# Kernel optimization log

Hardware: AMD Instinct MI355X
Metric: run time of the kernel (lower is better)

The kernel has to match this reference:

```python
import jax, jax.numpy as jnp
import numpy as np

EPS = 1e-12  # matches torch F.normalize default eps

def setup_inputs() -> dict:
    key = jax.random.key(0)
    k1, k2 = jax.random.split(key)
    n, d = 8192, 1024
    x = jax.random.normal(k1, (n, d), dtype=jnp.float32)
    weight = jax.random.normal(k2, (d, d), dtype=jnp.float32) * (2.0 / d) ** 0.5
    return {"x": x, "weight": weight}

def reference(x, weight):
    # L2-normalize rows (torch F.normalize, dim=1): x / max(||x||_2, eps)
    nrm = jnp.sqrt(jnp.sum(x * x, axis=1, keepdims=True))
    norm = x / jnp.maximum(nrm, EPS)
    # adjacency: cosine-similarity Gram matrix [n, n] (materialized as in source)
    adj = norm @ norm.T
    ax = adj @ x          # [n, d]
    axw = ax @ weight     # [n, d]
    return axw
```

## Files before the change

### kernel.cpp

```cpp
#include <hip/hip_runtime.h>
#include <stdint.h>

typedef unsigned short u16;
typedef unsigned int u32;
typedef __attribute__((ext_vector_type(8))) short short8;
typedef __attribute__((ext_vector_type(4))) float floatx4;

__device__ __forceinline__ u16 f2b(float f) {
    u32 u = __builtin_bit_cast(u32, f);
    return (u16)((u + 0x7fffu + ((u >> 16) & 1u)) >> 16);
}

__device__ __forceinline__ void gld16(const void* g, void* l) {
    __builtin_amdgcn_global_load_lds(
        (const __attribute__((address_space(1))) u32*)g,
        (__attribute__((address_space(3))) u32*)l, 16, 0, 0);
}

__global__ __launch_bounds__(256) void prep_norms(
    const float* __restrict__ x, float* __restrict__ rnorm, float* __restrict__ srnorm) {
    int row = blockIdx.x;
    int t = threadIdx.x;
    float4 v = ((const float4*)(x + (long)row * 1024))[t];
    float ss = v.x * v.x + v.y * v.y + v.z * v.z + v.w * v.w;
    #pragma unroll
    for (int off = 32; off > 0; off >>= 1) ss += __shfl_down(ss, off);
    __shared__ float red[4];
    if ((t & 63) == 0) red[t >> 6] = ss;
    __syncthreads();
    if (t == 0) {
        float r = 1.0f / fmaxf(sqrtf(red[0] + red[1] + red[2] + red[3]), 1e-12f);
        rnorm[row] = r;
        srnorm[row] = sqrtf(r);
    }
}

__global__ __launch_bounds__(256) void transpose_scale_dual(
    const float* __restrict__ src, const float* __restrict__ sr,
    u16* __restrict__ dstT, u16* __restrict__ dstR, int rows, int cols) {
    __shared__ float tile[64][65];
    __shared__ float rbuf[64];
    int r0 = blockIdx.x * 64, c0 = blockIdx.y * 64;
    int t = threadIdx.x;
    if (t < 64) rbuf[t] = (sr != nullptr) ? sr[r0 + t] : 1.0f;
    __syncthreads();
    #pragma unroll
    for (int i = 0; i < 4; i++) {
        int lin = i * 256 + t;
        int rr = lin >> 4, c4 = (lin & 15) << 2;
        float4 v = *(const float4*)(src + (long)(r0 + rr) * cols + c0 + c4);
        float s = rbuf[rr];
        v.x *= s; v.y *= s; v.z *= s; v.w *= s;
        tile[rr][c4] = v.x; tile[rr][c4 + 1] = v.y; tile[rr][c4 + 2] = v.z; tile[rr][c4 + 3] = v.w;
        if (dstR != nullptr) {
            ushort4 o; o.x = f2b(v.x); o.y = f2b(v.y); o.z = f2b(v.z); o.w = f2b(v.w);
            *(ushort4*)(dstR + (long)(r0 + rr) * cols + c0 + c4) = o;
        }
    }
    __syncthreads();
    #pragma unroll
    for (int i = 0; i < 4; i++) {
        int lin = i * 256 + t;
        int cc = lin >> 4, r4 = (lin & 15) << 2;
        ushort4 o;
        o.x = f2b(tile[r4][cc]);
        o.y = f2b(tile[r4 + 1][cc]);
        o.z = f2b(tile[r4 + 2][cc]);
        o.w = f2b(tile[r4 + 3][cc]);
        *(ushort4*)(dstT + (long)(c0 + cc) * rows + r0 + r4) = o;
    }
}

__global__ __launch_bounds__(256) void reduce_cast(
    const float* __restrict__ P, u16* __restrict__ D, int S, long E) {
    long i = ((long)blockIdx.x * 256 + threadIdx.x) * 4;
    float4 s = *(const float4*)(P + i);
    for (int z = 1; z < S; z++) {
        float4 v = *(const float4*)(P + z * E + i);
        s.x += v.x; s.y += v.y; s.z += v.z; s.w += v.w;
    }
    ushort4 o;
    o.x = f2b(s.x); o.y = f2b(s.y); o.z = f2b(s.z); o.w = f2b(s.w);
    *(ushort4*)(D + i) = o;
}

__global__ __launch_bounds__(256) void reduce_sym64(
    const float* __restrict__ P, u16* __restrict__ D, int S, long E) {
    __shared__ float lt[64][65];
    int ti = blockIdx.x >> 4, tj = blockIdx.x & 15;
    int t = threadIdx.x;
    int r = t >> 4, c4 = (t & 15) << 2;
    int kept = (ti <= 2 * (tj >> 1) + 1);
    if (kept) {
        #pragma unroll
        for (int it = 0; it < 4; it++) {
            int row = 64 * ti + it * 16 + r;
            long idx = (long)row * 1024 + 64 * tj + c4;
            float4 s = *(const float4*)(P + idx);
            for (int z = 1; z < S; z++) {
                float4 v = *(const float4*)(P + (long)z * E + idx);
                s.x += v.x; s.y += v.y; s.z += v.z; s.w += v.w;
            }
            ushort4 o; o.x = f2b(s.x); o.y = f2b(s.y); o.z = f2b(s.z); o.w = f2b(s.w);
            *(ushort4*)(D + idx) = o;
        }
    } else {
        #pragma unroll
        for (int it = 0; it < 4; it++) {
            int row = it * 16 + r;
            long idx = (long)(64 * tj + row) * 1024 + 64 * ti + c4;
            float4 s = *(const float4*)(P + idx);
            for (int z = 1; z < S; z++) {
                float4 v = *(const float4*)(P + (long)z * E + idx);
                s.x += v.x; s.y += v.y; s.z += v.z; s.w += v.w;
            }
            lt[row][c4] = s.x; lt[row][c4 + 1] = s.y; lt[row][c4 + 2] = s.z; lt[row][c4 + 3] = s.w;
        }
        __syncthreads();
        #pragma unroll
        for (int it = 0; it < 4; it++) {
            int dr = it * 16 + r;
            ushort4 o;
            o.x = f2b(lt[c4 + 0][dr]); o.y = f2b(lt[c4 + 1][dr]);
            o.z = f2b(lt[c4 + 2][dr]); o.w = f2b(lt[c4 + 3][dr]);
            *(ushort4*)(D + (long)(64 * ti + dr) * 1024 + 64 * tj + c4) = o;
        }
    }
}

__global__ __launch_bounds__(256, 4) void gemm64x128(
    const u16* __restrict__ A, const u16* __restrict__ B,
    float* __restrict__ C, const float* __restrict__ rowscale,
    int lda, int ldb, int ldc, int tilesN, int kIters, long coffz, int sym) {
    __shared__ __align__(16) u16 As[64 * 64];
    __shared__ __align__(16) u16 Bs[128 * 64];
    int tm, tn;
    if (sym) {
        int id = blockIdx.x, j = 0;
        while (true) {
            int c = (2 * j + 2 < 16) ? (2 * j + 2) : 16;
            if (id < c) break;
            id -= c; j++;
        }
        tn = j; tm = id;
    } else {
        tm = blockIdx.x / tilesN; tn = blockIdx.x % tilesN;
    }
    long kOff = (long)blockIdx.y * kIters * 64;
    const u16* Ap = A + (long)tm * 64 * lda + kOff;
    const u16* Bp = B + (long)tn * 128 * ldb + kOff;
    long coff = (long)blockIdx.y * coffz;

    int t = threadIdx.x;
    int lane = t & 63, w = t >> 6;
    int wm = (w & 1) * 32, wn = (w >> 1) * 64;
    int r16 = lane & 15, q = lane >> 4;

    int acl[2], bcl[4];
    #pragma unroll
    for (int j = 0; j < 2; j++) acl[j] = (w * 2 + j) * 64 + lane;
    #pragma unroll
    for (int j = 0; j < 4; j++) bcl[j] = (w * 4 + j) * 64 + lane;

    floatx4 acc[2][4];
    #pragma unroll
    for (int i = 0; i < 2; i++)
        #pragma unroll
        for (int j = 0; j < 4; j++) acc[i][j] = (floatx4){0.f, 0.f, 0.f, 0.f};

    for (int kt = 0; kt < kIters; kt++) {
        long kk = (long)kt * 64;
        #pragma unroll
        for (int j = 0; j < 2; j++) {
            int cl = acl[j], row = cl >> 3, cg = (cl & 7) ^ (row & 7);
            gld16(Ap + (long)row * lda + kk + cg * 8, (void*)&As[cl * 8]);
        }
        #pragma unroll
        for (int j = 0; j < 4; j++) {
            int cl = bcl[j], row = cl >> 3, cg = (cl & 7) ^ (row & 7);
            gld16(Bp + (long)row * ldb + kk + cg * 8, (void*)&Bs[cl * 8]);
        }
        __syncthreads();
        #pragma unroll
        for (int ks = 0; ks < 2; ks++) {
            short8 a[2], b[4];
            #pragma unroll
            for (int i = 0; i < 2; i++) {
                int rr = wm + i * 16 + r16;
                int cc = (ks * 4 + q) ^ (rr & 7);
                a[i] = *(const short8*)&As[rr * 64 + cc * 8];
            }
            #pragma unroll
            for (int j = 0; j < 4; j++) {
                int rr = wn + j * 16 + r16;
                int cc = (ks * 4 + q) ^ (rr & 7);
                b[j] = *(const short8*)&Bs[rr * 64 + cc * 8];
            }
            #pragma unroll
            for (int i = 0; i < 2; i++)
                #pragma unroll
                for (int j = 0; j < 4; j++)
                    acc[i][j] = __builtin_amdgcn_mfma_f32_16x16x32_bf16(a[i], b[j], acc[i][j], 0, 0, 0);
        }
        __syncthreads();
    }

    int m0 = tm * 64 + wm, n0 = tn * 128 + wn;
    #pragma unroll
    for (int i = 0; i < 2; i++) {
        int mm = m0 + i * 16 + q * 4;
        float rs[4];
        #pragma unroll
        for (int r = 0; r < 4; r++) rs[r] = (rowscale != nullptr) ? rowscale[mm + r] : 1.0f;
        #pragma unroll
        for (int j = 0; j < 4; j++) {
            int nn = n0 + j * 16 + r16;
            #pragma unroll
            for (int r = 0; r < 4; r++)
                C[coff + (long)(mm + r) * ldc + nn] = acc[i][j][r] * rs[r];
        }
    }
}

extern "C" void kernel_launch(void* const* d_in, const int* in_sizes, int n_in,
                              void* d_out, int out_size, void* d_ws, size_t ws_size,
                              hipStream_t stream) {
    const float* x = (const float*)d_in[0];
    const float* wgt = (const float*)d_in[1];
    float* out = (float*)d_out;
    char* ws = (char*)d_ws;

    const size_t MB = 1048576;
    float* rnorm  = (float*)ws;
    float* srnorm = (float*)(ws + 32768);
    u16*   YT     = (u16*)(ws + 65536);
    u16*   Yb     = (u16*)(ws + 65536 + 16 * MB);
    u16*   Wt     = (u16*)(ws + 65536 + 32 * MB);
    u16*   Gb     = (u16*)(ws + 65536 + 34 * MB);
    u16*   Mt     = (u16*)(ws + 65536 + 36 * MB);
    float* Gp     = (float*)(ws + 65536 + 38 * MB);
    float* Mp     = (float*)(ws + 65536 + 70 * MB);

    prep_norms<<<8192, 256, 0, stream>>>(x, rnorm, srnorm);
    transpose_scale_dual<<<dim3(128, 16), 256, 0, stream>>>(x, srnorm, YT, Yb, 8192, 1024);
    transpose_scale_dual<<<dim3(16, 16), 256, 0, stream>>>(wgt, nullptr, Wt, nullptr, 1024, 1024);
    gemm64x128<<<dim3(72, 8), 256, 0, stream>>>(YT, YT, Gp, nullptr,
                                                8192, 8192, 1024, 8, 16, 1048576, 1);
    reduce_sym64<<<256, 256, 0, stream>>>(Gp, Gb, 8, 1048576);
    gemm64x128<<<dim3(128, 2), 256, 0, stream>>>(Wt, Gb, Mp, nullptr,
                                                 1024, 1024, 1024, 8, 8, 1048576, 0);
    reduce_cast<<<1024, 256, 0, stream>>>(Mp, Mt, 2, 1048576);
    gemm64x128<<<dim3(1024, 1), 256, 0, stream>>>(Yb, Mt, out, srnorm,
                                                  1024, 1024, 1024, 8, 16, 0, 0);
}
```

Measured before the change: 168.1 us.

## Fuse norm prep, drop split-K reduce, add 128x128 final GEMM and block swizzle

Merges the row-norm pass and the transpose/scale pass into a single kernel that writes both the transposed sqrt-scaled Y and the fully normalized row-major Yn. The W·G GEMM no longer uses split-K: it writes bf16 output directly, so the separate reduce_cast kernel is removed. The final GEMM becomes a new 128x128-tile kernel with no row scale, since the rows are already fully normalized. Both GEMMs get a block-index remap over groups of 8, likely aiming at better distribution across the chip's XCDs and cache locality. The trade-offs are a W·G GEMM that now runs only 128 blocks, and the fused prep kernel reading x twice with just 256 blocks.

```diff
diff --git a/kernel.cpp b/kernel.cpp
--- a/kernel.cpp
+++ b/kernel.cpp
@@ -17,21 +17,55 @@
         (__attribute__((address_space(3))) u32*)l, 16, 0, 0);
 }
 
-__global__ __launch_bounds__(256) void prep_norms(
-    const float* __restrict__ x, float* __restrict__ rnorm, float* __restrict__ srnorm) {
-    int row = blockIdx.x;
-    int t = threadIdx.x;
-    float4 v = ((const float4*)(x + (long)row * 1024))[t];
-    float ss = v.x * v.x + v.y * v.y + v.z * v.z + v.w * v.w;
-    #pragma unroll
-    for (int off = 32; off > 0; off >>= 1) ss += __shfl_down(ss, off);
-    __shared__ float red[4];
-    if ((t & 63) == 0) red[t >> 6] = ss;
-    __syncthreads();
-    if (t == 0) {
-        float r = 1.0f / fmaxf(sqrtf(red[0] + red[1] + red[2] + red[3]), 1e-12f);
-        rnorm[row] = r;
-        srnorm[row] = sqrtf(r);
+__global__ __launch_bounds__(256) void fuse_prep(
+    const float* __restrict__ x, u16* __restrict__ YT, u16* __restrict__ Yn) {
+    __shared__ float tile[32][129];
+    int r0 = blockIdx.x * 32;
+    int t = threadIdx.x;
+    int tg = t >> 5, tl = t & 31;
+    float ss[4] = {0.f, 0.f, 0.f, 0.f};
+    for (int c = 0; c < 8; c++) {
+        #pragma unroll
+        for (int i = 0; i < 4; i++) {
+            int rr = i * 8 + tg;
+            float4 v = *(const float4*)(x + (long)(r0 + rr) * 1024 + c * 128 + tl * 4);
+            ss[i] += v.x * v.x + v.y * v.y + v.z * v.z + v.w * v.w;
+        }
+    }
+    float rs_[4], sr_[4];
+    #pragma unroll
+    for (int i = 0; i < 4; i++) {
+        #pragma unroll
+        for (int m = 16; m > 0; m >>= 1) ss[i] += __shfl_xor(ss[i], m);
+        float rcp = 1.0f / fmaxf(sqrtf(ss[i]), 1e-12f);
+        rs_[i] = rcp;
+        sr_[i] = sqrtf(rcp);
+    }
+    for (int c = 0; c < 8; c++) {
+        __syncthreads();
+        #pragma unroll
+        for (int i = 0; i < 4; i++) {
+            int rr = i * 8 + tg;
+            float4 v = *(const float4*)(x + (long)(r0 + rr) * 1024 + c * 128 + tl * 4);
+            ushort4 o;
+            o.x = f2b(v.x * rs_[i]); o.y = f2b(v.y * rs_[i]);
+            o.z = f2b(v.z * rs_[i]); o.w = f2b(v.w * rs_[i]);
+            *(ushort4*)(Yn + (long)(r0 + rr) * 1024 + c * 128 + tl * 4) = o;
+            tile[rr][tl * 4 + 0] = v.x * sr_[i];
+            tile[rr][tl * 4 + 1] = v.y * sr_[i];
+            tile[rr][tl * 4 + 2] = v.z * sr_[i];
+            tile[rr][tl * 4 + 3] = v.w * sr_[i];
+        }
+        __syncthreads();
+        #pragma unroll
+        for (int i = 0; i < 4; i++) {
+            int lin = i * 256 + t;
+            int cc = lin >> 3, r4 = (lin & 7) << 2;
+            ushort4 o;
+            o.x = f2b(tile[r4 + 0][cc]); o.y = f2b(tile[r4 + 1][cc]);
+            o.z = f2b(tile[r4 + 2][cc]); o.w = f2b(tile[r4 + 3][cc]);
+            *(ushort4*)(YT + (long)(c * 128 + cc) * 8192 + r0 + r4) = o;
+        }
     }
 }
 
@@ -71,19 +105,6 @@
     }
 }
 
-__global__ __launch_bounds__(256) void reduce_cast(
-    const float* __restrict__ P, u16* __restrict__ D, int S, long E) {
-    long i = ((long)blockIdx.x * 256 + threadIdx.x) * 4;
-    float4 s = *(const float4*)(P + i);
-    for (int z = 1; z < S; z++) {
-        float4 v = *(const float4*)(P + z * E + i);
-        s.x += v.x; s.y += v.y; s.z += v.z; s.w += v.w;
-    }
-    ushort4 o;
-    o.x = f2b(s.x); o.y = f2b(s.y); o.z = f2b(s.z); o.w = f2b(s.w);
-    *(ushort4*)(D + i) = o;
-}
-
 __global__ __launch_bounds__(256) void reduce_sym64(
     const float* __restrict__ P, u16* __restrict__ D, int S, long E) {
     __shared__ float lt[64][65];
@@ -131,12 +152,15 @@
 __global__ __launch_bounds__(256, 4) void gemm64x128(
     const u16* __restrict__ A, const u16* __restrict__ B,
     float* __restrict__ C, const float* __restrict__ rowscale,
-    int lda, int ldb, int ldc, int tilesN, int kIters, long coffz, int sym) {
+    int lda, int ldb, int ldc, int tilesN, int kIters, long coffz, int sym, int obf16) {
     __shared__ __align__(16) u16 As[64 * 64];
     __shared__ __align__(16) u16 Bs[128 * 64];
+    int bid = blockIdx.x;
+    int nx = gridDim.x;
+    if ((nx & 7) == 0) { int cpx = nx >> 3; bid = (bid & 7) * cpx + (bid >> 3); }
     int tm, tn;
     if (sym) {
-        int id = blockIdx.x, j = 0;
+        int id = bid, j = 0;
         while (true) {
             int c = (2 * j + 2 < 16) ? (2 * j + 2) : 16;
             if (id < c) break;
@@ -144,7 +168,7 @@
         }
         tn = j; tm = id;
     } else {
-        tm = blockIdx.x / tilesN; tn = blockIdx.x % tilesN;
+        tm = bid / tilesN; tn = bid % tilesN;
     }
     long kOff = (long)blockIdx.y * kIters * 64;
     const u16* Ap = A + (long)tm * 64 * lda + kOff;
@@ -216,8 +240,89 @@
         for (int j = 0; j < 4; j++) {
             int nn = n0 + j * 16 + r16;
             #pragma unroll
+            for (int r = 0; r < 4; r++) {
+                float v = acc[i][j][r] * rs[r];
+                if (obf16) ((u16*)C)[coff + (long)(mm + r) * ldc + nn] = f2b(v);
+                else       C[coff + (long)(mm + r) * ldc + nn] = v;
+            }
+        }
+    }
+}
+
+__global__ __launch_bounds__(256) void gemm128(
+    const u16* __restrict__ A, const u16* __restrict__ B,
+    float* __restrict__ C, const float* __restrict__ rowscale,
+    int lda, int ldb, int ldc, int tilesN, int kIters) {
+    __shared__ __align__(16) u16 As[128 * 64];
+    __shared__ __align__(16) u16 Bs[128 * 64];
+    int bid = blockIdx.x;
+    int nx = gridDim.x;
+    if ((nx & 7) == 0) { int cpx = nx >> 3; bid = (bid & 7) * cpx + (bid >> 3); }
+    int tm = bid / tilesN, tn = bid % tilesN;
+    const u16* Ap = A + (long)tm * 128 * lda;
+    const u16* Bp = B + (long)tn * 128 * ldb;
+
+    int t = threadIdx.x;
+    int lane = t & 63, w = t >> 6;
+    int wm = (w & 1) * 64, wn = (w >> 1) * 64;
+    int r16 = lane & 15, q = lane >> 4;
+
+    floatx4 acc[4][4];
+    #pragma unroll
+    for (int i = 0; i < 4; i++)
+        #pragma unroll
+        for (int j = 0; j < 4; j++) acc[i][j] = (floatx4){0.f, 0.f, 0.f, 0.f};
+
+    for (int kt = 0; kt < kIters; kt++) {
+        long kk = (long)kt * 64;
+        #pragma unroll
+        for (int j = 0; j < 4; j++) {
+            int cl = j * 256 + t, row = cl >> 3, cg = (cl & 7) ^ (row & 7);
+            gld16(Ap + (long)row * lda + kk + cg * 8, (void*)&As[cl * 8]);
+        }
+        #pragma unroll
+        for (int j = 0; j < 4; j++) {
+            int cl = j * 256 + t, row = cl >> 3, cg = (cl & 7) ^ (row & 7);
+            gld16(Bp + (long)row * ldb + kk + cg * 8, (void*)&Bs[cl * 8]);
+        }
+        __syncthreads();
+        #pragma unroll
+        for (int ks = 0; ks < 2; ks++) {
+            short8 a[4], b[4];
+            #pragma unroll
+            for (int i = 0; i < 4; i++) {
+                int rr = wm + i * 16 + r16;
+                int cc = (ks * 4 + q) ^ (rr & 7);
+                a[i] = *(const short8*)&As[rr * 64 + cc * 8];
+            }
+            #pragma unroll
+            for (int j = 0; j < 4; j++) {
+                int rr = wn + j * 16 + r16;
+                int cc = (ks * 4 + q) ^ (rr & 7);
+                b[j] = *(const short8*)&Bs[rr * 64 + cc * 8];
+            }
+            #pragma unroll
+            for (int i = 0; i < 4; i++)
+                #pragma unroll
+                for (int j = 0; j < 4; j++)
+                    acc[i][j] = __builtin_amdgcn_mfma_f32_16x16x32_bf16(a[i], b[j], acc[i][j], 0, 0, 0);
+        }
+        __syncthreads();
+    }
+
+    int m0 = tm * 128 + wm, n0 = tn * 128 + wn;
+    #pragma unroll
+    for (int i = 0; i < 4; i++) {
+        int mm = m0 + i * 16 + q * 4;
+        float rs[4];
+        #pragma unroll
+        for (int r = 0; r < 4; r++) rs[r] = (rowscale != nullptr) ? rowscale[mm + r] : 1.0f;
+        #pragma unroll
+        for (int j = 0; j < 4; j++) {
+            int nn = n0 + j * 16 + r16;
+            #pragma unroll
             for (int r = 0; r < 4; r++)
-                C[coff + (long)(mm + r) * ldc + nn] = acc[i][j][r] * rs[r];
+                C[(long)(mm + r) * ldc + nn] = acc[i][j][r] * rs[r];
         }
     }
 }
@@ -231,25 +336,20 @@
     char* ws = (char*)d_ws;
 
     const size_t MB = 1048576;
-    float* rnorm  = (float*)ws;
-    float* srnorm = (float*)(ws + 32768);
-    u16*   YT     = (u16*)(ws + 65536);
-    u16*   Yb     = (u16*)(ws + 65536 + 16 * MB);
-    u16*   Wt     = (u16*)(ws + 65536 + 32 * MB);
-    u16*   Gb     = (u16*)(ws + 65536 + 34 * MB);
-    u16*   Mt     = (u16*)(ws + 65536 + 36 * MB);
-    float* Gp     = (float*)(ws + 65536 + 38 * MB);
-    float* Mp     = (float*)(ws + 65536 + 70 * MB);
-
-    prep_norms<<<8192, 256, 0, stream>>>(x, rnorm, srnorm);
-    transpose_scale_dual<<<dim3(128, 16), 256, 0, stream>>>(x, srnorm, YT, Yb, 8192, 1024);
+    u16*   YT = (u16*)ws;
+    u16*   Yn = (u16*)(ws + 16 * MB);
+    u16*   Wt = (u16*)(ws + 32 * MB);
+    u16*   Gb = (u16*)(ws + 34 * MB);
+    u16*   Mt = (u16*)(ws + 36 * MB);
+    float* Gp = (float*)(ws + 38 * MB);
+
+    fuse_prep<<<256, 256, 0, stream>>>(x, YT, Yn);
     transpose_scale_dual<<<dim3(16, 16), 256, 0, stream>>>(wgt, nullptr, Wt, nullptr, 1024, 1024);
     gemm64x128<<<dim3(72, 8), 256, 0, stream>>>(YT, YT, Gp, nullptr,
-                                                8192, 8192, 1024, 8, 16, 1048576, 1);
+                                                8192, 8192, 1024, 8, 16, 1048576, 1, 0);
     reduce_sym64<<<256, 256, 0, stream>>>(Gp, Gb, 8, 1048576);
-    gemm64x128<<<dim3(128, 2), 256, 0, stream>>>(Wt, Gb, Mp, nullptr,
-                                                 1024, 1024, 1024, 8, 8, 1048576, 0);
-    reduce_cast<<<1024, 256, 0, stream>>>(Mp, Mt, 2, 1048576);
-    gemm64x128<<<dim3(1024, 1), 256, 0, stream>>>(Yb, Mt, out, srnorm,
-                                                  1024, 1024, 1024, 8, 16, 0, 0);
-}
+    gemm64x128<<<dim3(128, 1), 256, 0, stream>>>(Wt, Gb, (float*)Mt, nullptr,
+                                                 1024, 1024, 1024, 8, 16, 0, 0, 1);
+    gemm128<<<dim3(512, 1), 256, 0, stream>>>(Yn, Mt, out, nullptr,
+                                              1024, 1024, 1024, 8, 16);
+}
```

Measured after the change: 170.6 us. About the same (+1.5%).
